# Kernel tuning notes

Measured on AMD Instinct MI355X. Metric: run time of the kernel, lower is better.

## Reference

```python
import jax, jax.numpy as jnp
import numpy as np

RES = 128
RES_V = RES + 1          # dense vertex grid resolution
N_VOX = 400000           # active sparse voxels
SDF_BIAS = -1.0 / RES
CUBE_CORNERS = jnp.array([[0,0,0],[1,0,0],[0,1,0],[1,1,0],
                          [0,0,1],[1,0,1],[0,1,1],[1,1,1]], dtype=jnp.int32)


def setup_inputs() -> dict:
    key = jax.random.key(0)
    k1, k2 = jax.random.split(key)
    coords = jax.random.randint(k1, (N_VOX, 3), 0, RES, dtype=jnp.int32)
    feats = jax.random.normal(k2, (N_VOX, 101), dtype=jnp.float32)
    return {"coords": coords, "feats": feats}


def reference(coords, feats):
    N = feats.shape[0]
    # layout: sdf[0:8] deform[8:32] weights[32:53] color[53:101]
    sdf = feats[:, 0:8].reshape(N, 8, 1) + SDF_BIAS
    deform = feats[:, 8:32].reshape(N, 8, 3)
    weights = feats[:, 32:53]                      # [N,21]
    color = feats[:, 53:101].reshape(N, 8, 6)
    value = jnp.concatenate([sdf, deform, color], axis=-1)   # [N,8,10]

    # cube-corner vertex ids on the dense (RES_V)^3 grid; identical to
    # torch.unique dedup + scatter_reduce(mean) + get_dense_attrs scatter.
    corner = coords[:, None, :] + CUBE_CORNERS[None]         # [N,8,3]
    vid = ((corner[..., 0] * RES_V + corner[..., 1]) * RES_V
           + corner[..., 2]).reshape(-1)                     # [N*8]
    n_verts = RES_V ** 3

    sums = jax.ops.segment_sum(value.reshape(-1, 10), vid, num_segments=n_verts)
    cnts = jax.ops.segment_sum(jnp.ones((N * 8,), feats.dtype), vid,
                               num_segments=n_verts)
    v_attrs = sums / jnp.maximum(cnts, 1.0)[:, None]         # mean, 0 if untouched

    sdf_d = v_attrs[:, 0]
    deform_d = v_attrs[:, 1:4]
    colors_d = v_attrs[:, 4:10]

    # regular dense vertex positions + tanh-bounded deformation
    vertsid = jnp.arange(n_verts)
    reg_v = jnp.stack([vertsid // (RES_V ** 2),
                       (vertsid // RES_V) % RES_V,
                       vertsid % RES_V], axis=1).astype(feats.dtype)
    x_nx3 = reg_v / RES - 0.5 + (1.0 - 1e-8) / (2.0 * RES) * jnp.tanh(deform_d)

    # dense flexicube weights grid (scatter-set at active voxels)
    cid = (coords[:, 0] * RES + coords[:, 1]) * RES + coords[:, 2]
    weights_d = jnp.zeros((RES ** 3, 21), feats.dtype).at[cid].set(weights)

    # [n_verts, 10]: deformed positions (3) | sdf (1) | colors+normals (6)
    v_out = jnp.concatenate([x_nx3, sdf_d[:, None], colors_d], axis=-1)
    return (v_out, weights_d)
```

## Files before the change

kernel.cpp:

```cpp
#include <hip/hip_runtime.h>

#define RES 128
#define RES_V 129
#define N_VOX 400000

constexpr int N_VERTS = RES_V * RES_V * RES_V;
constexpr int N_CELLS = RES * RES * RES;
constexpr long VOUT_WORDS = (long)N_VERTS * 10;
constexpr long OUTW_WORDS = (long)N_CELLS * 21;
constexpr int SCAN_BLOCKS = 512;
constexpr int GATHER_BLOCKS = (N_VERTS + 255) / 256;
constexpr float SDF_BIAS = -1.0f / 128.0f;
constexpr float DEFORM_SCALE = (float)((1.0 - 1e-8) / 256.0);
constexpr float INV_RES = 1.0f / 128.0f;

static __device__ __forceinline__ unsigned int f2bf(float x) {
    unsigned int u = __float_as_uint(x);
    unsigned int r = ((u >> 16) & 1u) + 0x7FFFu;
    return (u + r) >> 16;
}
static __device__ __forceinline__ float bf_lo(unsigned int w) {
    return __uint_as_float(w << 16);
}
static __device__ __forceinline__ float bf_hi(unsigned int w) {
    return __uint_as_float(w & 0xFFFF0000u);
}

__global__ void __launch_bounds__(256) init_counts(unsigned int* __restrict__ counts)
{
    int t = blockIdx.x * blockDim.x + threadIdx.x;
    if (t < N_CELLS) counts[t] = 0u;
}

__global__ void __launch_bounds__(256) count_kernel(const int* __restrict__ coords,
                                                    unsigned int* __restrict__ counts)
{
    int n = blockIdx.x * blockDim.x + threadIdx.x;
    if (n >= N_VOX) return;
    int cx = coords[n * 3 + 0];
    int cy = coords[n * 3 + 1];
    int cz = coords[n * 3 + 2];
    int cid = (cx * RES + cy) * RES + cz;
    atomicAdd(counts + cid, 1u);
}

__global__ void __launch_bounds__(256) scan1_kernel(const unsigned int* __restrict__ counts,
                                                    unsigned int* __restrict__ packed,
                                                    unsigned int* __restrict__ blocksums)
{
    __shared__ unsigned int part[256];
    int b = blockIdx.x, t = threadIdx.x;
    long base = (long)b * 4096 + (long)t * 16;
    unsigned int v[16], s = 0;
#pragma unroll
    for (int i = 0; i < 16; ++i) { v[i] = counts[base + i]; s += v[i]; }
    part[t] = s;
    __syncthreads();
    for (int off = 1; off < 256; off <<= 1) {
        unsigned int x = (t >= off) ? part[t - off] : 0u;
        __syncthreads();
        part[t] += x;
        __syncthreads();
    }
    unsigned int excl = (t == 0) ? 0u : part[t - 1];
    if (t == 255) blocksums[b] = part[255];
    unsigned int run = excl;
#pragma unroll
    for (int i = 0; i < 16; ++i) { packed[base + i] = run; run += v[i]; }
}

__global__ void __launch_bounds__(256) fixup2_kernel(unsigned int* __restrict__ packed,
                                                     unsigned int* __restrict__ cnt_cursor,
                                                     const unsigned int* __restrict__ blocksums)
{
    __shared__ unsigned int red[256];
    int t = threadIdx.x;
    int cell0 = blockIdx.x * 256;
    int R = cell0 >> 12;
    unsigned int part = 0;
    for (int j = t; j < R; j += 256) part += blocksums[j];
    red[t] = part;
    __syncthreads();
    for (int off = 128; off > 0; off >>= 1) {
        if (t < off) red[t] += red[t + off];
        __syncthreads();
    }
    unsigned int P = red[0];
    int cell = cell0 + t;
    unsigned int g = packed[cell] + P;
    unsigned int cnt = cnt_cursor[cell];
    packed[cell] = g | (min(cnt, 255u) << 24);
    cnt_cursor[cell] = g;
    if (cell == 0) packed[N_CELLS] = (unsigned int)N_VOX;
}

__global__ void __launch_bounds__(256) fill_kernel(const int* __restrict__ coords,
                                                   unsigned int* __restrict__ cursors,
                                                   unsigned int* __restrict__ list)
{
    int n = blockIdx.x * blockDim.x + threadIdx.x;
    if (n >= N_VOX) return;
    int cx = coords[n * 3 + 0];
    int cy = coords[n * 3 + 1];
    int cz = coords[n * 3 + 2];
    int cid = (cx * RES + cy) * RES + cz;
    unsigned int slot = atomicAdd(cursors + cid, 1u);
    list[slot] = (unsigned int)n;
}

__global__ void __launch_bounds__(256) permute_kernel(const float* __restrict__ feats,
                                                      const unsigned int* __restrict__ list,
                                                      unsigned int* __restrict__ perm)
{
    int g = blockIdx.x * blockDim.x + threadIdx.x;
    int slot = g >> 3;
    int c = g & 7;
    if (slot >= N_VOX) return;
    long src = (long)list[slot] * 101;
    float v[10];
    v[0] = feats[src + c];
#pragma unroll
    for (int k = 0; k < 3; ++k) v[1 + k] = feats[src + 8 + 3 * c + k];
#pragma unroll
    for (int k = 0; k < 6; ++k) v[4 + k] = feats[src + 53 + 6 * c + k];
    unsigned int* d = perm + (long)slot * 40 + c * 5;
#pragma unroll
    for (int q = 0; q < 5; ++q)
        d[q] = f2bf(v[2 * q]) | (f2bf(v[2 * q + 1]) << 16);
}

__global__ void __launch_bounds__(256) gather_perm(const unsigned int* __restrict__ packed,
                                                   const unsigned int* __restrict__ perm,
                                                   float* __restrict__ vout)
{
    const int nwg = GATHER_BLOCKS;
    const int q = nwg / 8, r = nwg % 8;
    int bid = blockIdx.x;
    int xcd = bid % 8, i = bid / 8;
    int wg = (xcd < r ? xcd * (q + 1) : r * (q + 1) + (xcd - r) * q) + i;
    int vid = wg * 256 + threadIdx.x;
    if (vid >= N_VERTS) return;

    int z = vid % RES_V;
    int tmp = vid / RES_V;
    int y = tmp % RES_V;
    int x = tmp / RES_V;

    float sums[10];
#pragma unroll
    for (int j = 0; j < 10; ++j) sums[j] = 0.0f;
    int cnt = 0;

#pragma unroll
    for (int dx = 0; dx < 2; ++dx) {
        int cx = x - dx;
        if ((unsigned)cx >= RES) continue;
#pragma unroll
        for (int dy = 0; dy < 2; ++dy) {
            int cy = y - dy;
            if ((unsigned)cy >= RES) continue;
#pragma unroll
            for (int dz = 0; dz < 2; ++dz) {
                int cz = z - dz;
                if ((unsigned)cz >= RES) continue;
                int cid = (cx * RES + cy) * RES + cz;
                unsigned int w = packed[cid];
                unsigned int cc = w >> 24;
                if (cc == 0u) continue;
                unsigned int s = w & 0xFFFFFFu;
                unsigned int e = (cc == 255u) ? (packed[cid + 1] & 0xFFFFFFu)
                                              : s + cc;
                int c = dx + 2 * dy + 4 * dz;
                for (unsigned int ii = s; ii < e; ++ii) {
                    const unsigned int* b = perm + (long)ii * 40 + c * 5;
                    unsigned int w0 = b[0], w1 = b[1], w2 = b[2], w3 = b[3], w4 = b[4];
                    sums[0] += bf_lo(w0); sums[1] += bf_hi(w0);
                    sums[2] += bf_lo(w1); sums[3] += bf_hi(w1);
                    sums[4] += bf_lo(w2); sums[5] += bf_hi(w2);
                    sums[6] += bf_lo(w3); sums[7] += bf_hi(w3);
                    sums[8] += bf_lo(w4); sums[9] += bf_hi(w4);
                }
                cnt += (int)(e - s);
            }
        }
    }

    float fc = (float)cnt;
    float inv = 1.0f / fmaxf(fc, 1.0f);
    float o[10];
    o[0] = (float)x * INV_RES - 0.5f + DEFORM_SCALE * tanhf(sums[1] * inv);
    o[1] = (float)y * INV_RES - 0.5f + DEFORM_SCALE * tanhf(sums[2] * inv);
    o[2] = (float)z * INV_RES - 0.5f + DEFORM_SCALE * tanhf(sums[3] * inv);
    o[3] = (sums[0] + fc * SDF_BIAS) * inv;
#pragma unroll
    for (int j = 0; j < 6; ++j) o[4 + j] = sums[4 + j] * inv;

    float* p = vout + (long)vid * 10;
#pragma unroll
    for (int j = 0; j < 5; ++j)
        *(float2*)(p + 2 * j) = make_float2(o[2 * j], o[2 * j + 1]);
}

__global__ void __launch_bounds__(256) weights_fill2(const float* __restrict__ feats,
                                                     const unsigned int* __restrict__ packed,
                                                     const unsigned int* __restrict__ list,
                                                     float* __restrict__ outw)
{
    __shared__ float vals[256 * 21];
    int t = threadIdx.x;
    int cell0 = blockIdx.x * 256;
    int cell = cell0 + t;

    unsigned int w = packed[cell];
    unsigned int cc = w >> 24;
    if (cc > 0u) {
        unsigned int s = w & 0xFFFFFFu;
        unsigned int e = (cc == 255u) ? (packed[cell + 1] & 0xFFFFFFu) : s + cc;
        unsigned int li = 0u;
        for (unsigned int i = s; i < e; ++i) li = max(li, list[i]);
        const float* f = feats + (long)li * 101 + 32;
#pragma unroll
        for (int j = 0; j < 21; ++j) vals[t * 21 + j] = f[j];
    } else {
#pragma unroll
        for (int j = 0; j < 21; ++j) vals[t * 21 + j] = 0.0f;
    }
    __syncthreads();

    float* dst = outw + (long)cell0 * 21;
#pragma unroll
    for (int k = 0; k < 21; ++k) dst[t + 256 * k] = vals[t + 256 * k];
}

extern "C" void kernel_launch(void* const* d_in, const int* in_sizes, int n_in,
                              void* d_out, int out_size, void* d_ws, size_t ws_size,
                              hipStream_t stream) {
    const int* coords = (const int*)d_in[0];
    const float* feats = (const float*)d_in[1];
    float* out = (float*)d_out;
    float* vout = out;
    float* outw = out + VOUT_WORDS;

    unsigned int* packed = (unsigned int*)d_ws;
    unsigned int* list = packed + (N_CELLS + 1);
    unsigned int* blocksums = list + N_VOX;

    unsigned int* perm = (unsigned int*)outw;
    unsigned int* cnt_cursor = (unsigned int*)(outw + (OUTW_WORDS - N_CELLS - 16));

    init_counts<<<(N_CELLS + 255) / 256, 256, 0, stream>>>(cnt_cursor);
    count_kernel<<<(N_VOX + 255) / 256, 256, 0, stream>>>(coords, cnt_cursor);
    scan1_kernel<<<SCAN_BLOCKS, 256, 0, stream>>>(cnt_cursor, packed, blocksums);
    fixup2_kernel<<<N_CELLS / 256, 256, 0, stream>>>(packed, cnt_cursor, blocksums);
    fill_kernel<<<(N_VOX + 255) / 256, 256, 0, stream>>>(coords, cnt_cursor, list);
    permute_kernel<<<(N_VOX * 8 + 255) / 256, 256, 0, stream>>>(feats, list, perm);
    gather_perm<<<GATHER_BLOCKS, 256, 0, stream>>>(packed, perm, vout);
    weights_fill2<<<N_CELLS / 256, 256, 0, stream>>>(feats, packed, list, outw);
}
```

Baseline: 227.0 us.

## Fuse fill and permute kernels; gather two z-adjacent vertices per thread

Merges the slot-allocation fill kernel with the bf16 permute kernel: one lane per voxel takes the atomic slot and broadcasts it to the other seven lanes via shuffle, so feats are read directly by voxel index and one launch disappears. The vertex gather kernel now handles two consecutive z vertices per thread, so the shared middle cell's packed entry is loaded once and contributes to both outputs. This cuts launch overhead and redundant index loads, but doubles per-thread accumulator registers, drops the XCD-aware block remapping, and makes the output write pattern less uniform.

```diff
diff --git a/kernel.cpp b/kernel.cpp
--- a/kernel.cpp
+++ b/kernel.cpp
@@ -9,7 +9,9 @@
 constexpr long VOUT_WORDS = (long)N_VERTS * 10;
 constexpr long OUTW_WORDS = (long)N_CELLS * 21;
 constexpr int SCAN_BLOCKS = 512;
-constexpr int GATHER_BLOCKS = (N_VERTS + 255) / 256;
+constexpr int COLS = RES_V * RES_V;
+constexpr int ZPAIRS = 65;
+constexpr long GTHREADS = (long)COLS * ZPAIRS;
 constexpr float SDF_BIAS = -1.0f / 128.0f;
 constexpr float DEFORM_SCALE = (float)((1.0 - 1e-8) / 256.0);
 constexpr float INV_RES = 1.0f / 128.0f;
@@ -24,6 +26,17 @@
 }
 static __device__ __forceinline__ float bf_hi(unsigned int w) {
     return __uint_as_float(w & 0xFFFF0000u);
+}
+
+static __device__ __forceinline__ void acc_row(const unsigned int* __restrict__ perm,
+                                               long ii, int c, float* sums) {
+    const unsigned int* b = perm + ii * 40 + c * 5;
+    unsigned int w0 = b[0], w1 = b[1], w2 = b[2], w3 = b[3], w4 = b[4];
+    sums[0] += bf_lo(w0); sums[1] += bf_hi(w0);
+    sums[2] += bf_lo(w1); sums[3] += bf_hi(w1);
+    sums[4] += bf_lo(w2); sums[5] += bf_hi(w2);
+    sums[6] += bf_lo(w3); sums[7] += bf_hi(w3);
+    sums[8] += bf_lo(w4); sums[9] += bf_hi(w4);
 }
 
 __global__ void __launch_bounds__(256) init_counts(unsigned int* __restrict__ counts)
@@ -94,62 +107,58 @@
     if (cell == 0) packed[N_CELLS] = (unsigned int)N_VOX;
 }
 
-__global__ void __launch_bounds__(256) fill_kernel(const int* __restrict__ coords,
-                                                   unsigned int* __restrict__ cursors,
-                                                   unsigned int* __restrict__ list)
-{
-    int n = blockIdx.x * blockDim.x + threadIdx.x;
-    if (n >= N_VOX) return;
+__global__ void __launch_bounds__(256) fillperm_kernel(const int* __restrict__ coords,
+                                                       const float* __restrict__ feats,
+                                                       unsigned int* __restrict__ cursors,
+                                                       unsigned int* __restrict__ list,
+                                                       unsigned int* __restrict__ perm)
+{
+    int g = blockIdx.x * blockDim.x + threadIdx.x;
+    int n = g >> 3;
+    int c = g & 7;
     int cx = coords[n * 3 + 0];
     int cy = coords[n * 3 + 1];
     int cz = coords[n * 3 + 2];
     int cid = (cx * RES + cy) * RES + cz;
-    unsigned int slot = atomicAdd(cursors + cid, 1u);
-    list[slot] = (unsigned int)n;
-}
-
-__global__ void __launch_bounds__(256) permute_kernel(const float* __restrict__ feats,
-                                                      const unsigned int* __restrict__ list,
-                                                      unsigned int* __restrict__ perm)
-{
-    int g = blockIdx.x * blockDim.x + threadIdx.x;
-    int slot = g >> 3;
-    int c = g & 7;
-    if (slot >= N_VOX) return;
-    long src = (long)list[slot] * 101;
+    unsigned int slot = 0;
+    if (c == 0) {
+        slot = atomicAdd(cursors + cid, 1u);
+        list[slot] = (unsigned int)n;
+    }
+    int lane = threadIdx.x & 63;
+    slot = __shfl(slot, lane & ~7);
+
+    const float* f = feats + (long)n * 101;
     float v[10];
-    v[0] = feats[src + c];
-#pragma unroll
-    for (int k = 0; k < 3; ++k) v[1 + k] = feats[src + 8 + 3 * c + k];
-#pragma unroll
-    for (int k = 0; k < 6; ++k) v[4 + k] = feats[src + 53 + 6 * c + k];
+    v[0] = f[c];
+#pragma unroll
+    for (int k = 0; k < 3; ++k) v[1 + k] = f[8 + 3 * c + k];
+#pragma unroll
+    for (int k = 0; k < 6; ++k) v[4 + k] = f[53 + 6 * c + k];
     unsigned int* d = perm + (long)slot * 40 + c * 5;
 #pragma unroll
     for (int q = 0; q < 5; ++q)
         d[q] = f2bf(v[2 * q]) | (f2bf(v[2 * q + 1]) << 16);
 }
 
-__global__ void __launch_bounds__(256) gather_perm(const unsigned int* __restrict__ packed,
-                                                   const unsigned int* __restrict__ perm,
-                                                   float* __restrict__ vout)
-{
-    const int nwg = GATHER_BLOCKS;
-    const int q = nwg / 8, r = nwg % 8;
-    int bid = blockIdx.x;
-    int xcd = bid % 8, i = bid / 8;
-    int wg = (xcd < r ? xcd * (q + 1) : r * (q + 1) + (xcd - r) * q) + i;
-    int vid = wg * 256 + threadIdx.x;
-    if (vid >= N_VERTS) return;
-
-    int z = vid % RES_V;
-    int tmp = vid / RES_V;
-    int y = tmp % RES_V;
-    int x = tmp / RES_V;
-
-    float sums[10];
-#pragma unroll
-    for (int j = 0; j < 10; ++j) sums[j] = 0.0f;
-    int cnt = 0;
+__global__ void __launch_bounds__(256) gather2_kernel(const unsigned int* __restrict__ packed,
+                                                      const unsigned int* __restrict__ perm,
+                                                      float* __restrict__ vout)
+{
+    long t = (long)blockIdx.x * blockDim.x + threadIdx.x;
+    if (t >= GTHREADS) return;
+    int col = (int)(t / ZPAIRS);
+    int rem = (int)(t - (long)col * ZPAIRS);
+    int x = col / RES_V;
+    int y = col - x * RES_V;
+    int z0 = rem * 2;
+    int z1 = z0 + 1;
+    bool has1 = z1 < RES_V;
+
+    float s0[10], s1[10];
+#pragma unroll
+    for (int j = 0; j < 10; ++j) { s0[j] = 0.0f; s1[j] = 0.0f; }
+    int c0 = 0, c1 = 0;
 
 #pragma unroll
     for (int dx = 0; dx < 2; ++dx) {
@@ -159,46 +168,79 @@
         for (int dy = 0; dy < 2; ++dy) {
             int cy = y - dy;
             if ((unsigned)cy >= RES) continue;
-#pragma unroll
-            for (int dz = 0; dz < 2; ++dz) {
-                int cz = z - dz;
-                if ((unsigned)cz >= RES) continue;
-                int cid = (cx * RES + cy) * RES + cz;
-                unsigned int w = packed[cid];
+            int cbase = (cx * RES + cy) * RES;
+            int cxy = dx + 2 * dy;
+
+            int czA = z0 - 1;
+            if ((unsigned)czA < RES) {
+                unsigned int w = packed[cbase + czA];
                 unsigned int cc = w >> 24;
-                if (cc == 0u) continue;
-                unsigned int s = w & 0xFFFFFFu;
-                unsigned int e = (cc == 255u) ? (packed[cid + 1] & 0xFFFFFFu)
-                                              : s + cc;
-                int c = dx + 2 * dy + 4 * dz;
-                for (unsigned int ii = s; ii < e; ++ii) {
-                    const unsigned int* b = perm + (long)ii * 40 + c * 5;
-                    unsigned int w0 = b[0], w1 = b[1], w2 = b[2], w3 = b[3], w4 = b[4];
-                    sums[0] += bf_lo(w0); sums[1] += bf_hi(w0);
-                    sums[2] += bf_lo(w1); sums[3] += bf_hi(w1);
-                    sums[4] += bf_lo(w2); sums[5] += bf_hi(w2);
-                    sums[6] += bf_lo(w3); sums[7] += bf_hi(w3);
-                    sums[8] += bf_lo(w4); sums[9] += bf_hi(w4);
+                if (cc) {
+                    unsigned int s = w & 0xFFFFFFu;
+                    unsigned int e = (cc == 255u) ? (packed[cbase + czA + 1] & 0xFFFFFFu) : s + cc;
+                    for (unsigned int ii = s; ii < e; ++ii) acc_row(perm, (long)ii, cxy + 4, s0);
+                    c0 += (int)(e - s);
                 }
-                cnt += (int)(e - s);
+            }
+            if (z0 < RES) {
+                unsigned int w = packed[cbase + z0];
+                unsigned int cc = w >> 24;
+                if (cc) {
+                    unsigned int s = w & 0xFFFFFFu;
+                    unsigned int e = (cc == 255u) ? (packed[cbase + z0 + 1] & 0xFFFFFFu) : s + cc;
+                    for (unsigned int ii = s; ii < e; ++ii) {
+                        acc_row(perm, (long)ii, cxy, s0);
+                        if (has1) acc_row(perm, (long)ii, cxy + 4, s1);
+                    }
+                    c0 += (int)(e - s);
+                    if (has1) c1 += (int)(e - s);
+                }
+            }
+            if (has1 && z1 < RES) {
+                unsigned int w = packed[cbase + z1];
+                unsigned int cc = w >> 24;
+                if (cc) {
+                    unsigned int s = w & 0xFFFFFFu;
+                    unsigned int e = (cc == 255u) ? (packed[cbase + z1 + 1] & 0xFFFFFFu) : s + cc;
+                    for (unsigned int ii = s; ii < e; ++ii) acc_row(perm, (long)ii, cxy, s1);
+                    c1 += (int)(e - s);
+                }
             }
         }
     }
 
-    float fc = (float)cnt;
-    float inv = 1.0f / fmaxf(fc, 1.0f);
-    float o[10];
-    o[0] = (float)x * INV_RES - 0.5f + DEFORM_SCALE * tanhf(sums[1] * inv);
-    o[1] = (float)y * INV_RES - 0.5f + DEFORM_SCALE * tanhf(sums[2] * inv);
-    o[2] = (float)z * INV_RES - 0.5f + DEFORM_SCALE * tanhf(sums[3] * inv);
-    o[3] = (sums[0] + fc * SDF_BIAS) * inv;
-#pragma unroll
-    for (int j = 0; j < 6; ++j) o[4 + j] = sums[4 + j] * inv;
-
-    float* p = vout + (long)vid * 10;
-#pragma unroll
-    for (int j = 0; j < 5; ++j)
-        *(float2*)(p + 2 * j) = make_float2(o[2 * j], o[2 * j + 1]);
+    {
+        float fc = (float)c0;
+        float inv = 1.0f / fmaxf(fc, 1.0f);
+        float o[10];
+        o[0] = (float)x * INV_RES - 0.5f + DEFORM_SCALE * tanhf(s0[1] * inv);
+        o[1] = (float)y * INV_RES - 0.5f + DEFORM_SCALE * tanhf(s0[2] * inv);
+        o[2] = (float)z0 * INV_RES - 0.5f + DEFORM_SCALE * tanhf(s0[3] * inv);
+        o[3] = (s0[0] + fc * SDF_BIAS) * inv;
+#pragma unroll
+        for (int j = 0; j < 6; ++j) o[4 + j] = s0[4 + j] * inv;
+        long vid = ((long)col) * RES_V + z0;
+        float* p = vout + vid * 10;
+#pragma unroll
+        for (int j = 0; j < 5; ++j)
+            *(float2*)(p + 2 * j) = make_float2(o[2 * j], o[2 * j + 1]);
+    }
+    if (has1) {
+        float fc = (float)c1;
+        float inv = 1.0f / fmaxf(fc, 1.0f);
+        float o[10];
+        o[0] = (float)x * INV_RES - 0.5f + DEFORM_SCALE * tanhf(s1[1] * inv);
+        o[1] = (float)y * INV_RES - 0.5f + DEFORM_SCALE * tanhf(s1[2] * inv);
+        o[2] = (float)z1 * INV_RES - 0.5f + DEFORM_SCALE * tanhf(s1[3] * inv);
+        o[3] = (s1[0] + fc * SDF_BIAS) * inv;
+#pragma unroll
+        for (int j = 0; j < 6; ++j) o[4 + j] = s1[4 + j] * inv;
+        long vid = ((long)col) * RES_V + z1;
+        float* p = vout + vid * 10;
+#pragma unroll
+        for (int j = 0; j < 5; ++j)
+            *(float2*)(p + 2 * j) = make_float2(o[2 * j], o[2 * j + 1]);
+    }
 }
 
 __global__ void __launch_bounds__(256) weights_fill2(const float* __restrict__ feats,
@@ -252,8 +294,7 @@
     count_kernel<<<(N_VOX + 255) / 256, 256, 0, stream>>>(coords, cnt_cursor);
     scan1_kernel<<<SCAN_BLOCKS, 256, 0, stream>>>(cnt_cursor, packed, blocksums);
     fixup2_kernel<<<N_CELLS / 256, 256, 0, stream>>>(packed, cnt_cursor, blocksums);
-    fill_kernel<<<(N_VOX + 255) / 256, 256, 0, stream>>>(coords, cnt_cursor, list);
-    permute_kernel<<<(N_VOX * 8 + 255) / 256, 256, 0, stream>>>(feats, list, perm);
-    gather_perm<<<GATHER_BLOCKS, 256, 0, stream>>>(packed, perm, vout);
+    fillperm_kernel<<<(N_VOX * 8) / 256, 256, 0, stream>>>(coords, feats, cnt_cursor, list, perm);
+    gather2_kernel<<<(int)((GTHREADS + 255) / 256), 256, 0, stream>>>(packed, perm, vout);
     weights_fill2<<<N_CELLS / 256, 256, 0, stream>>>(feats, packed, list, outw);
 }
```

Result: no change. 230.3 us (+1.4%).

## Pre-aggregate duplicate voxels per cell and vectorize padded bf16 perm rows

Applied to the files above, without the earlier changes.

Adds an aggregate kernel that sums all duplicate voxels of a cell into that cell's first permuted row. The vertex gather then reads exactly one row per neighbouring cell instead of running a variable-length loop. Perm rows are padded from 40 to 48 words so each corner's data can be read with uint2 vector loads. The init kernel becomes hipMemsetAsync, the XCD block remapping in the gather is dropped, and the weights fill gets a fast path for single-voxel cells. The cost is an extra launch that scans every cell, and the pre-summed values are rounded to bf16 a second time, which adds a small precision loss.

```diff
diff --git a/kernel.cpp b/kernel.cpp
--- a/kernel.cpp
+++ b/kernel.cpp
@@ -26,10 +26,17 @@
     return __uint_as_float(w & 0xFFFF0000u);
 }
 
-__global__ void __launch_bounds__(256) init_counts(unsigned int* __restrict__ counts)
-{
-    int t = blockIdx.x * blockDim.x + threadIdx.x;
-    if (t < N_CELLS) counts[t] = 0u;
+static __device__ __forceinline__ void acc_row(const unsigned int* __restrict__ perm,
+                                               long ii, int c, float* sums) {
+    const unsigned int* b = perm + ii * 48 + c * 6;
+    uint2 p01 = *(const uint2*)(b);
+    uint2 p23 = *(const uint2*)(b + 2);
+    unsigned int w4 = b[4];
+    sums[0] += bf_lo(p01.x); sums[1] += bf_hi(p01.x);
+    sums[2] += bf_lo(p01.y); sums[3] += bf_hi(p01.y);
+    sums[4] += bf_lo(p23.x); sums[5] += bf_hi(p23.x);
+    sums[6] += bf_lo(p23.y); sums[7] += bf_hi(p23.y);
+    sums[8] += bf_lo(w4);    sums[9] += bf_hi(w4);
 }
 
 __global__ void __launch_bounds__(256) count_kernel(const int* __restrict__ coords,
@@ -123,24 +130,50 @@
     for (int k = 0; k < 3; ++k) v[1 + k] = feats[src + 8 + 3 * c + k];
 #pragma unroll
     for (int k = 0; k < 6; ++k) v[4 + k] = feats[src + 53 + 6 * c + k];
-    unsigned int* d = perm + (long)slot * 40 + c * 5;
-#pragma unroll
-    for (int q = 0; q < 5; ++q)
-        d[q] = f2bf(v[2 * q]) | (f2bf(v[2 * q + 1]) << 16);
+    unsigned int* d = perm + (long)slot * 48 + c * 6;
+    unsigned int w0 = f2bf(v[0]) | (f2bf(v[1]) << 16);
+    unsigned int w1 = f2bf(v[2]) | (f2bf(v[3]) << 16);
+    unsigned int w2 = f2bf(v[4]) | (f2bf(v[5]) << 16);
+    unsigned int w3 = f2bf(v[6]) | (f2bf(v[7]) << 16);
+    unsigned int w4 = f2bf(v[8]) | (f2bf(v[9]) << 16);
+    *(uint2*)(d)     = make_uint2(w0, w1);
+    *(uint2*)(d + 2) = make_uint2(w2, w3);
+    d[4] = w4;
+}
+
+__global__ void __launch_bounds__(256) aggregate_kernel(const unsigned int* __restrict__ packed,
+                                                        unsigned int* __restrict__ perm)
+{
+    int cell = blockIdx.x * blockDim.x + threadIdx.x;
+    unsigned int w = packed[cell];
+    unsigned int cc = w >> 24;
+    if (cc < 2u) return;
+    unsigned int s = w & 0xFFFFFFu;
+    unsigned int e = (cc == 255u) ? (packed[cell + 1] & 0xFFFFFFu) : s + cc;
+#pragma unroll
+    for (int c = 0; c < 8; ++c) {
+        float a[10];
+#pragma unroll
+        for (int j = 0; j < 10; ++j) a[j] = 0.0f;
+        for (unsigned int r = s; r < e; ++r) acc_row(perm, (long)r, c, a);
+        unsigned int* d = perm + (long)s * 48 + c * 6;
+        unsigned int w0 = f2bf(a[0]) | (f2bf(a[1]) << 16);
+        unsigned int w1 = f2bf(a[2]) | (f2bf(a[3]) << 16);
+        unsigned int w2 = f2bf(a[4]) | (f2bf(a[5]) << 16);
+        unsigned int w3 = f2bf(a[6]) | (f2bf(a[7]) << 16);
+        unsigned int w4 = f2bf(a[8]) | (f2bf(a[9]) << 16);
+        *(uint2*)(d)     = make_uint2(w0, w1);
+        *(uint2*)(d + 2) = make_uint2(w2, w3);
+        d[4] = w4;
+    }
 }
 
 __global__ void __launch_bounds__(256) gather_perm(const unsigned int* __restrict__ packed,
                                                    const unsigned int* __restrict__ perm,
                                                    float* __restrict__ vout)
 {
-    const int nwg = GATHER_BLOCKS;
-    const int q = nwg / 8, r = nwg % 8;
-    int bid = blockIdx.x;
-    int xcd = bid % 8, i = bid / 8;
-    int wg = (xcd < r ? xcd * (q + 1) : r * (q + 1) + (xcd - r) * q) + i;
-    int vid = wg * 256 + threadIdx.x;
+    int vid = blockIdx.x * blockDim.x + threadIdx.x;
     if (vid >= N_VERTS) return;
-
     int z = vid % RES_V;
     int tmp = vid / RES_V;
     int y = tmp % RES_V;
@@ -168,19 +201,9 @@
                 unsigned int cc = w >> 24;
                 if (cc == 0u) continue;
                 unsigned int s = w & 0xFFFFFFu;
-                unsigned int e = (cc == 255u) ? (packed[cid + 1] & 0xFFFFFFu)
-                                              : s + cc;
-                int c = dx + 2 * dy + 4 * dz;
-                for (unsigned int ii = s; ii < e; ++ii) {
-                    const unsigned int* b = perm + (long)ii * 40 + c * 5;
-                    unsigned int w0 = b[0], w1 = b[1], w2 = b[2], w3 = b[3], w4 = b[4];
-                    sums[0] += bf_lo(w0); sums[1] += bf_hi(w0);
-                    sums[2] += bf_lo(w1); sums[3] += bf_hi(w1);
-                    sums[4] += bf_lo(w2); sums[5] += bf_hi(w2);
-                    sums[6] += bf_lo(w3); sums[7] += bf_hi(w3);
-                    sums[8] += bf_lo(w4); sums[9] += bf_hi(w4);
-                }
-                cnt += (int)(e - s);
+                if (cc == 255u) cnt += (int)((packed[cid + 1] & 0xFFFFFFu) - s);
+                else cnt += (int)cc;
+                acc_row(perm, (long)s, dx + 2 * dy + 4 * dz, sums);
             }
         }
     }
@@ -215,9 +238,14 @@
     unsigned int cc = w >> 24;
     if (cc > 0u) {
         unsigned int s = w & 0xFFFFFFu;
-        unsigned int e = (cc == 255u) ? (packed[cell + 1] & 0xFFFFFFu) : s + cc;
-        unsigned int li = 0u;
-        for (unsigned int i = s; i < e; ++i) li = max(li, list[i]);
+        unsigned int li;
+        if (cc == 1u) {
+            li = list[s];
+        } else {
+            unsigned int e = (cc == 255u) ? (packed[cell + 1] & 0xFFFFFFu) : s + cc;
+            li = 0u;
+            for (unsigned int i = s; i < e; ++i) li = max(li, list[i]);
+        }
         const float* f = feats + (long)li * 101 + 32;
 #pragma unroll
         for (int j = 0; j < 21; ++j) vals[t * 21 + j] = f[j];
@@ -248,12 +276,13 @@
     unsigned int* perm = (unsigned int*)outw;
     unsigned int* cnt_cursor = (unsigned int*)(outw + (OUTW_WORDS - N_CELLS - 16));
 
-    init_counts<<<(N_CELLS + 255) / 256, 256, 0, stream>>>(cnt_cursor);
+    hipMemsetAsync(cnt_cursor, 0, sizeof(unsigned int) * (size_t)N_CELLS, stream);
     count_kernel<<<(N_VOX + 255) / 256, 256, 0, stream>>>(coords, cnt_cursor);
     scan1_kernel<<<SCAN_BLOCKS, 256, 0, stream>>>(cnt_cursor, packed, blocksums);
     fixup2_kernel<<<N_CELLS / 256, 256, 0, stream>>>(packed, cnt_cursor, blocksums);
     fill_kernel<<<(N_VOX + 255) / 256, 256, 0, stream>>>(coords, cnt_cursor, list);
     permute_kernel<<<(N_VOX * 8 + 255) / 256, 256, 0, stream>>>(feats, list, perm);
+    aggregate_kernel<<<N_CELLS / 256, 256, 0, stream>>>(packed, perm);
     gather_perm<<<GATHER_BLOCKS, 256, 0, stream>>>(packed, perm, vout);
     weights_fill2<<<N_CELLS / 256, 256, 0, stream>>>(feats, packed, list, outw);
 }
```

Result: slower. 276.9 us (+21.9%).
